# Performance work log

Measured on AMD Instinct MI355X. Metric: run time of the kernel, lower is better.

Reference implementation:

```python
import jax, jax.numpy as jnp
import numpy as np

# icosphere level 6
NV = 40962   # vertices
NF = 81920   # faces
B = 16
CIN = 32
COUT = 32
NCOEFF = 4


def _spmm(rows, cols, vals, nrows, x):
    """Sparse (COO) @ dense over the vertex/face axis.
    x: [B, C, N] -> out: [B, C, nrows].
    """
    # gather columns, scale by nonzero values, scatter-add into rows
    g = x.transpose(2, 0, 1)[cols] * vals[:, None, None]   # [nnz, B, C]
    out = jax.ops.segment_sum(g, rows, num_segments=nrows)  # [nrows, B, C]
    return out.transpose(1, 2, 0)                           # [B, C, nrows]


def setup_inputs() -> dict:
    key = jax.random.key(0)
    ks = jax.random.split(key, 10)
    x = jax.random.normal(ks[0], (B, CIN, NV), dtype=jnp.float32)

    # G: [3*NF, NV], 3 nnz per row (3 vertices per face), component-major rows
    g_nnz = 3 * NF * 3
    G_rows = jnp.repeat(jnp.arange(3 * NF, dtype=jnp.int32), 3)
    G_cols = jax.random.randint(ks[1], (g_nnz,), 0, NV, dtype=jnp.int32)
    G_vals = jax.random.normal(ks[2], (g_nnz,), dtype=jnp.float32) * 0.5

    # L: [NV, NV], ~7 nnz per row (vertex valence + self)
    l_nnz = NV * 7
    L_rows = jnp.repeat(jnp.arange(NV, dtype=jnp.int32), 7)
    L_cols = jax.random.randint(ks[3], (l_nnz,), 0, NV, dtype=jnp.int32)
    L_vals = jax.random.normal(ks[4], (l_nnz,), dtype=jnp.float32) * 0.5

    # F2V: [NV, NF], ~6 faces per vertex, averaging weights
    f_nnz = NV * 6
    F2V_rows = jnp.repeat(jnp.arange(NV, dtype=jnp.int32), 6)
    F2V_cols = jax.random.randint(ks[5], (f_nnz,), 0, NF, dtype=jnp.int32)
    F2V_vals = jnp.full((f_nnz,), 1.0 / 6.0, dtype=jnp.float32)

    # per-face east-west / north-south tangent vectors: [NF, 3]
    EW = jax.random.normal(ks[6], (NF, 3), dtype=jnp.float32)
    NS = jax.random.normal(ks[7], (NF, 3), dtype=jnp.float32)

    stdv = 1.0 / np.sqrt(CIN * NCOEFF)
    coeffs = jax.random.uniform(ks[8], (COUT, CIN, NCOEFF), dtype=jnp.float32,
                                minval=-stdv, maxval=stdv)
    bias = jax.random.uniform(ks[9], (COUT,), dtype=jnp.float32,
                              minval=-stdv, maxval=stdv)

    return {
        "x": x,
        "G_rows": G_rows, "G_cols": G_cols, "G_vals": G_vals,
        "L_rows": L_rows, "L_cols": L_cols, "L_vals": L_vals,
        "F2V_rows": F2V_rows, "F2V_cols": F2V_cols, "F2V_vals": F2V_vals,
        "EW": EW, "NS": NS,
        "coeffs": coeffs, "bias": bias,
    }


def reference(x, G_rows, G_cols, G_vals, L_rows, L_cols, L_vals,
              F2V_rows, F2V_cols, F2V_vals, EW, NS, coeffs, bias):
    b, c, nv = x.shape
    # gradient on faces: [B,C,3*NF] -> [B,C,3,NF] -> [B,C,NF,3]
    grad_face = _spmm(G_rows, G_cols, G_vals, 3 * NF, x)
    grad_face = grad_face.reshape(b, c, 3, NF).transpose(0, 1, 3, 2)
    # Laplacian on vertices (stride=1 -> nv_prev = nv)
    laplacian = _spmm(L_rows, L_cols, L_vals, NV, x)
    identity = x  # x[..., :nv_prev] with nv_prev == nv
    # project face gradients onto EW / NS frames
    grad_face_ew = jnp.sum(grad_face * EW, axis=-1)  # [B,C,NF]
    grad_face_ns = jnp.sum(grad_face * NS, axis=-1)
    # average back to vertices
    grad_vert_ew = _spmm(F2V_rows, F2V_cols, F2V_vals, NV, grad_face_ew)
    grad_vert_ns = _spmm(F2V_rows, F2V_cols, F2V_vals, NV, grad_face_ns)
    # combine 4 features with learned per-channel coefficients
    feat = jnp.stack([identity, laplacian, grad_vert_ew, grad_vert_ns], axis=-1)  # [B,C,NV,4]
    out = jnp.einsum('bcnk,ock->bon', feat, coeffs) + bias[:, None]
    return out
```

## Files before the change

### kernel.cpp

```cpp
#include <hip/hip_runtime.h>
#include <hip/hip_bf16.h>

#define NVERT 40962
#define NFACE 81920
#define GRID_V ((NVERT + 3) / 4)
#define GRID_F (NFACE / 4)

typedef unsigned int uint;
typedef __attribute__((ext_vector_type(4))) uint  uintx4;
typedef __attribute__((ext_vector_type(4))) float floatx4;
typedef __attribute__((ext_vector_type(8))) short shortx8;

__device__ __forceinline__ uint packbf2(float a, float b) {
  uint ua = __float_as_uint(a); ua = ua + 0x7fffu + ((ua >> 16) & 1u);
  uint ub = __float_as_uint(b); ub = ub + 0x7fffu + ((ub >> 16) & 1u);
  return (ua >> 16) | (ub & 0xffff0000u);
}
__device__ __forceinline__ float2 unpackbf2(uint u) {
  float2 r;
  r.x = __uint_as_float(u << 16);
  r.y = __uint_as_float(u & 0xffff0000u);
  return r;
}
__device__ __forceinline__ short bfr(float x) {
  uint u = __float_as_uint(x);
  u = u + 0x7fffu + ((u >> 16) & 1u);
  return (short)(u >> 16);
}

__device__ __forceinline__ int swz(int blk, int nwg) {
  int q = nwg >> 3, r = nwg & 7;
  int xcd = blk & 7, idx = blk >> 3;
  return (xcd < r ? xcd * (q + 1) : r * (q + 1) + (xcd - r) * q) + idx;
}

__global__ __launch_bounds__(256) void k_transpose(const float* __restrict__ x,
                                                   uint* __restrict__ xT) {
  __shared__ float tile[32][33];
  int n0 = blockIdx.x * 32;
  int r0 = blockIdx.y * 32;
  int tx = threadIdx.x & 31;
  int ty = threadIdx.x >> 5;
#pragma unroll
  for (int i = 0; i < 32; i += 8) {
    int n = n0 + tx;
    tile[ty + i][tx] = (n < NVERT)
        ? __builtin_nontemporal_load(&x[(size_t)(r0 + ty + i) * NVERT + n]) : 0.f;
  }
  __syncthreads();
#pragma unroll
  for (int i = 0; i < 32; i += 16) {
    int nl = (threadIdx.x >> 4) + i;
    int u  = threadIdx.x & 15;
    int n  = n0 + nl;
    int ug = 16 * blockIdx.y + u;
    int up = (ug & 3) * 64 + (ug >> 4) * 4 + ((ug >> 2) & 3);
    if (n < NVERT)
      xT[(size_t)n * 256 + up] = packbf2(tile[2 * u][nl], tile[2 * u + 1][nl]);
  }
}

__global__ __launch_bounds__(256) void k_prepw(const float* __restrict__ coeffs,
                                               short* __restrict__ wsW) {
  int t = threadIdx.x;
  int ks = t >> 6, lane = t & 63;
  int bm = lane & 15, h = lane >> 4;
  const float* wp0 = coeffs + (size_t)bm * 128 + 32 * ks + 8 * h;
  shortx8 f0, f1;
#pragma unroll
  for (int j = 0; j < 8; ++j) {
    f0[j] = bfr(wp0[j]);
    f1[j] = bfr(wp0[16 * 128 + j]);
  }
  *(shortx8*)(wsW + ((size_t)(ks * 2 + 0) * 64 + lane) * 8) = f0;
  *(shortx8*)(wsW + ((size_t)(ks * 2 + 1) * 64 + lane) * 8) = f1;
}

__global__ __launch_bounds__(256) void k_faces(
    const uint* __restrict__ xT,
    const int* __restrict__ Gc, const float* __restrict__ Gv,
    const float* __restrict__ EW, const float* __restrict__ NS,
    uint* __restrict__ gf) {
  const int t = threadIdx.x, lane = t & 63;
  const int f = __builtin_amdgcn_readfirstlane(swz(blockIdx.x, GRID_F) * 4 + (t >> 6));
  const int voff = 4 * lane;

  float ea[4][2], sa[4][2];
#pragma unroll
  for (int ks = 0; ks < 4; ++ks) {
    ea[ks][0] = 0.f; ea[ks][1] = 0.f;
    sa[ks][0] = 0.f; sa[ks][1] = 0.f;
  }

#pragma unroll
  for (int comp = 0; comp < 3; ++comp) {
    const int base = comp * (3 * NFACE) + 3 * f;
    const float ewc = EW[3 * f + comp];
    const float nsc = NS[3 * f + comp];
#pragma unroll
    for (int j = 0; j < 3; ++j) {
      const int col = Gc[base + j];
      const float v = Gv[base + j];
      const float ve = v * ewc, vn = v * nsc;
      uintx4 g = *(const uintx4*)(xT + (size_t)col * 256 + voff);
#pragma unroll
      for (int ks = 0; ks < 4; ++ks) {
        float2 p = unpackbf2(g[ks]);
        ea[ks][0] = fmaf(ve, p.x, ea[ks][0]); ea[ks][1] = fmaf(ve, p.y, ea[ks][1]);
        sa[ks][0] = fmaf(vn, p.x, sa[ks][0]); sa[ks][1] = fmaf(vn, p.y, sa[ks][1]);
      }
    }
  }
  uintx4 we, wn;
#pragma unroll
  for (int ks = 0; ks < 4; ++ks) {
    we[ks] = packbf2(ea[ks][0], ea[ks][1]);
    wn[ks] = packbf2(sa[ks][0], sa[ks][1]);
  }
  uint* op = gf + (size_t)f * 512 + voff;
  *(uintx4*)op         = we;
  *(uintx4*)(op + 256) = wn;
}

__global__ __launch_bounds__(256) void k_verts(
    const uint* __restrict__ xT,
    const int* __restrict__ Lc, const float* __restrict__ Lv,
    const int* __restrict__ Fc, const float* __restrict__ Fv,
    const uint* __restrict__ gf,
    const short* __restrict__ wsW, const float* __restrict__ bias,
    float* __restrict__ out) {
  const int t = threadIdx.x, lane = t & 63;
  const int n = __builtin_amdgcn_readfirstlane(swz(blockIdx.x, GRID_V) * 4 + (t >> 6));
  if (n >= NVERT) return;
  const int h = lane >> 4, bm = lane & 15;
  const int voff = 4 * lane;

  uintx4 idw = *(const uintx4*)(xT + (size_t)n * 256 + voff);

  float lap[4][2];
#pragma unroll
  for (int ks = 0; ks < 4; ++ks) { lap[ks][0] = 0.f; lap[ks][1] = 0.f; }
#pragma unroll
  for (int j = 0; j < 7; ++j) {
    const int col = Lc[7 * n + j];
    const float v = Lv[7 * n + j];
    uintx4 g = *(const uintx4*)(xT + (size_t)col * 256 + voff);
#pragma unroll
    for (int ks = 0; ks < 4; ++ks) {
      float2 p = unpackbf2(g[ks]);
      lap[ks][0] = fmaf(v, p.x, lap[ks][0]);
      lap[ks][1] = fmaf(v, p.y, lap[ks][1]);
    }
  }

  float ea[4][2], na[4][2];
#pragma unroll
  for (int ks = 0; ks < 4; ++ks) {
    ea[ks][0] = 0.f; ea[ks][1] = 0.f;
    na[ks][0] = 0.f; na[ks][1] = 0.f;
  }
#pragma unroll
  for (int j = 0; j < 6; ++j) {
    const int fc = Fc[6 * n + j];
    const float v = Fv[6 * n + j];
    const uint* rp = gf + (size_t)fc * 512 + voff;
    uintx4 ge = *(const uintx4*)rp;
    uintx4 gn = *(const uintx4*)(rp + 256);
#pragma unroll
    for (int ks = 0; ks < 4; ++ks) {
      float2 a = unpackbf2(ge[ks]);
      float2 b = unpackbf2(gn[ks]);
      ea[ks][0] = fmaf(v, a.x, ea[ks][0]); ea[ks][1] = fmaf(v, a.y, ea[ks][1]);
      na[ks][0] = fmaf(v, b.x, na[ks][0]); na[ks][1] = fmaf(v, b.y, na[ks][1]);
    }
  }

  shortx8 afr[4];
#pragma unroll
  for (int ks = 0; ks < 4; ++ks) {
    float2 ip = unpackbf2(idw[ks]);
    shortx8 a;
    a[0] = bfr(ip.x);      a[1] = bfr(lap[ks][0]);
    a[2] = bfr(ea[ks][0]); a[3] = bfr(na[ks][0]);
    a[4] = bfr(ip.y);      a[5] = bfr(lap[ks][1]);
    a[6] = bfr(ea[ks][1]); a[7] = bfr(na[ks][1]);
    afr[ks] = a;
  }

  float b0 = bias[bm], b1 = bias[16 + bm];
  floatx4 acc0 = {b0, b0, b0, b0};
  floatx4 acc1 = {b1, b1, b1, b1};
#pragma unroll
  for (int ks = 0; ks < 4; ++ks) {
    shortx8 bf0 = *(const shortx8*)(wsW + ((size_t)(ks * 2 + 0) * 64 + lane) * 8);
    acc0 = __builtin_amdgcn_mfma_f32_16x16x32_bf16(afr[ks], bf0, acc0, 0, 0, 0);
    shortx8 bf1 = *(const shortx8*)(wsW + ((size_t)(ks * 2 + 1) * 64 + lane) * 8);
    acc1 = __builtin_amdgcn_mfma_f32_16x16x32_bf16(afr[ks], bf1, acc1, 0, 0, 0);
  }

#pragma unroll
  for (int reg = 0; reg < 4; ++reg) {
    int b = h * 4 + reg;
    out[(size_t)(b * 32 + bm) * NVERT + n]      = acc0[reg];
    out[(size_t)(b * 32 + 16 + bm) * NVERT + n] = acc1[reg];
  }
}

extern "C" void kernel_launch(void* const* d_in, const int* in_sizes, int n_in,
                              void* d_out, int out_size, void* d_ws, size_t ws_size,
                              hipStream_t stream) {
  const float* x      = (const float*)d_in[0];
  const int*   Gc     = (const int*)  d_in[2];
  const float* Gv     = (const float*)d_in[3];
  const int*   Lc     = (const int*)  d_in[5];
  const float* Lv     = (const float*)d_in[6];
  const int*   Fc     = (const int*)  d_in[8];
  const float* Fv     = (const float*)d_in[9];
  const float* EW     = (const float*)d_in[10];
  const float* NS     = (const float*)d_in[11];
  const float* coeffs = (const float*)d_in[12];
  const float* bias   = (const float*)d_in[13];
  float* out = (float*)d_out;

  uint* xT  = (uint*)d_ws;
  uint* gf  = xT + (size_t)NVERT * 256;
  short* wsW = (short*)(gf + (size_t)NFACE * 512);

  dim3 gT((NVERT + 31) / 32, 16);
  k_transpose<<<gT, 256, 0, stream>>>(x, xT);
  k_prepw<<<1, 256, 0, stream>>>(coeffs, wsW);
  k_faces<<<GRID_F, 256, 0, stream>>>(xT, Gc, Gv, EW, NS, gf);
  k_verts<<<GRID_V, 256, 0, stream>>>(xT, Lc, Lv, Fc, Fv, gf, wsW, bias, out);
}
```

Measured before the change: 479.4 us.

## Compose face-to-vertex and gradient operators into per-vertex gather weights

```diff
diff --git a/kernel.cpp b/kernel.cpp
--- a/kernel.cpp
+++ b/kernel.cpp
@@ -4,7 +4,6 @@
 #define NVERT 40962
 #define NFACE 81920
 #define GRID_V ((NVERT + 3) / 4)
-#define GRID_F (NFACE / 4)
 
 typedef unsigned int uint;
 typedef __attribute__((ext_vector_type(4))) uint  uintx4;
@@ -76,57 +75,38 @@
   *(shortx8*)(wsW + ((size_t)(ks * 2 + 1) * 64 + lane) * 8) = f1;
 }
 
-__global__ __launch_bounds__(256) void k_faces(
-    const uint* __restrict__ xT,
+__global__ __launch_bounds__(256) void k_prep(
+    const int* __restrict__ Fc, const float* __restrict__ Fv,
     const int* __restrict__ Gc, const float* __restrict__ Gv,
     const float* __restrict__ EW, const float* __restrict__ NS,
-    uint* __restrict__ gf) {
-  const int t = threadIdx.x, lane = t & 63;
-  const int f = __builtin_amdgcn_readfirstlane(swz(blockIdx.x, GRID_F) * 4 + (t >> 6));
-  const int voff = 4 * lane;
-
-  float ea[4][2], sa[4][2];
-#pragma unroll
-  for (int ks = 0; ks < 4; ++ks) {
-    ea[ks][0] = 0.f; ea[ks][1] = 0.f;
-    sa[ks][0] = 0.f; sa[ks][1] = 0.f;
-  }
-
+    int* __restrict__ cols, float* __restrict__ wew, float* __restrict__ wns) {
+  int idx = blockIdx.x * 256 + threadIdx.x;
+  if (idx >= NVERT * 6) return;
+  int n = idx / 6, j = idx - 6 * n;
+  int f = Fc[idx];
+  float wv = Fv[idx];
+  int bo = n * 64 + j * 9;
 #pragma unroll
   for (int comp = 0; comp < 3; ++comp) {
-    const int base = comp * (3 * NFACE) + 3 * f;
-    const float ewc = EW[3 * f + comp];
-    const float nsc = NS[3 * f + comp];
-#pragma unroll
-    for (int j = 0; j < 3; ++j) {
-      const int col = Gc[base + j];
-      const float v = Gv[base + j];
-      const float ve = v * ewc, vn = v * nsc;
-      uintx4 g = *(const uintx4*)(xT + (size_t)col * 256 + voff);
-#pragma unroll
-      for (int ks = 0; ks < 4; ++ks) {
-        float2 p = unpackbf2(g[ks]);
-        ea[ks][0] = fmaf(ve, p.x, ea[ks][0]); ea[ks][1] = fmaf(ve, p.y, ea[ks][1]);
-        sa[ks][0] = fmaf(vn, p.x, sa[ks][0]); sa[ks][1] = fmaf(vn, p.y, sa[ks][1]);
-      }
+    float e = wv * EW[3 * f + comp];
+    float s = wv * NS[3 * f + comp];
+    int gb = 3 * (comp * NFACE + f);
+#pragma unroll
+    for (int k = 0; k < 3; ++k) {
+      int   c  = Gc[gb + k];
+      float gv = Gv[gb + k];
+      cols[bo + comp * 3 + k] = c;
+      wew[bo + comp * 3 + k]  = e * gv;
+      wns[bo + comp * 3 + k]  = s * gv;
     }
   }
-  uintx4 we, wn;
-#pragma unroll
-  for (int ks = 0; ks < 4; ++ks) {
-    we[ks] = packbf2(ea[ks][0], ea[ks][1]);
-    wn[ks] = packbf2(sa[ks][0], sa[ks][1]);
-  }
-  uint* op = gf + (size_t)f * 512 + voff;
-  *(uintx4*)op         = we;
-  *(uintx4*)(op + 256) = wn;
-}
-
-__global__ __launch_bounds__(256) void k_verts(
+}
+
+__global__ __launch_bounds__(256) void k_vfused(
     const uint* __restrict__ xT,
     const int* __restrict__ Lc, const float* __restrict__ Lv,
-    const int* __restrict__ Fc, const float* __restrict__ Fv,
-    const uint* __restrict__ gf,
+    const int* __restrict__ cols, const float* __restrict__ wew,
+    const float* __restrict__ wns,
     const short* __restrict__ wsW, const float* __restrict__ bias,
     float* __restrict__ out) {
   const int t = threadIdx.x, lane = t & 63;
@@ -159,19 +139,20 @@
     ea[ks][0] = 0.f; ea[ks][1] = 0.f;
     na[ks][0] = 0.f; na[ks][1] = 0.f;
   }
-#pragma unroll
-  for (int j = 0; j < 6; ++j) {
-    const int fc = Fc[6 * n + j];
-    const float v = Fv[6 * n + j];
-    const uint* rp = gf + (size_t)fc * 512 + voff;
-    uintx4 ge = *(const uintx4*)rp;
-    uintx4 gn = *(const uintx4*)(rp + 256);
+  const int*   cb = cols + (size_t)n * 64;
+  const float* eb = wew  + (size_t)n * 64;
+  const float* nb = wns  + (size_t)n * 64;
+#pragma unroll 6
+  for (int j = 0; j < 54; ++j) {
+    const int   c  = cb[j];
+    const float ve = eb[j];
+    const float vn = nb[j];
+    uintx4 g = *(const uintx4*)(xT + (size_t)c * 256 + voff);
 #pragma unroll
     for (int ks = 0; ks < 4; ++ks) {
-      float2 a = unpackbf2(ge[ks]);
-      float2 b = unpackbf2(gn[ks]);
-      ea[ks][0] = fmaf(v, a.x, ea[ks][0]); ea[ks][1] = fmaf(v, a.y, ea[ks][1]);
-      na[ks][0] = fmaf(v, b.x, na[ks][0]); na[ks][1] = fmaf(v, b.y, na[ks][1]);
+      float2 p = unpackbf2(g[ks]);
+      ea[ks][0] = fmaf(ve, p.x, ea[ks][0]); ea[ks][1] = fmaf(ve, p.y, ea[ks][1]);
+      na[ks][0] = fmaf(vn, p.x, na[ks][0]); na[ks][1] = fmaf(vn, p.y, na[ks][1]);
     }
   }
 
@@ -222,13 +203,17 @@
   const float* bias   = (const float*)d_in[13];
   float* out = (float*)d_out;
 
-  uint* xT  = (uint*)d_ws;
-  uint* gf  = xT + (size_t)NVERT * 256;
-  short* wsW = (short*)(gf + (size_t)NFACE * 512);
+  uint*  xT   = (uint*)d_ws;
+  int*   cols = (int*)(xT + (size_t)NVERT * 256);
+  float* wewT = (float*)(cols + (size_t)NVERT * 64);
+  float* wnsT = wewT + (size_t)NVERT * 64;
+  short* wsW  = (short*)(wnsT + (size_t)NVERT * 64);
 
   dim3 gT((NVERT + 31) / 32, 16);
   k_transpose<<<gT, 256, 0, stream>>>(x, xT);
   k_prepw<<<1, 256, 0, stream>>>(coeffs, wsW);
-  k_faces<<<GRID_F, 256, 0, stream>>>(xT, Gc, Gv, EW, NS, gf);
-  k_verts<<<GRID_V, 256, 0, stream>>>(xT, Lc, Lv, Fc, Fv, gf, wsW, bias, out);
-}
+  k_prep<<<(NVERT * 6 + 255) / 256, 256, 0, stream>>>(Fc, Fv, Gc, Gv, EW, NS,
+                                                      cols, wewT, wnsT);
+  k_vfused<<<GRID_V, 256, 0, stream>>>(xT, Lc, Lv, cols, wewT, wnsT,
+                                       wsW, bias, out);
+}
```

Measured after the change: 589.9 us. +23.0%, slower.

## Split batch into two chunks so per-pass gather working sets fit in cache

Applied to the files above, without the earlier changes.

```diff
diff --git a/kernel.cpp b/kernel.cpp
--- a/kernel.cpp
+++ b/kernel.cpp
@@ -3,8 +3,9 @@
 
 #define NVERT 40962
 #define NFACE 81920
-#define GRID_V ((NVERT + 3) / 4)
-#define GRID_F (NFACE / 4)
+#define NPAIR_V 20481
+#define GRID_VP 5121
+#define GRID_FP 10240
 
 typedef unsigned int uint;
 typedef __attribute__((ext_vector_type(4))) uint  uintx4;
@@ -33,6 +34,7 @@
   int xcd = blk & 7, idx = blk >> 3;
   return (xcd < r ? xcd * (q + 1) : r * (q + 1) + (xcd - r) * q) + idx;
 }
+
 
 __global__ __launch_bounds__(256) void k_transpose(const float* __restrict__ x,
                                                    uint* __restrict__ xT) {
@@ -54,9 +56,11 @@
     int u  = threadIdx.x & 15;
     int n  = n0 + nl;
     int ug = 16 * blockIdx.y + u;
-    int up = (ug & 3) * 64 + (ug >> 4) * 4 + ((ug >> 2) & 3);
+    int chunk = ug >> 7;
+    int q = ((ug & 3) * 8 + ((ug >> 4) & 7)) * 4 + ((ug >> 2) & 3);
     if (n < NVERT)
-      xT[(size_t)n * 256 + up] = packbf2(tile[2 * u][nl], tile[2 * u + 1][nl]);
+      xT[(size_t)chunk * NVERT * 128 + (size_t)n * 128 + q] =
+          packbf2(tile[2 * u][nl], tile[2 * u + 1][nl]);
   }
 }
 
@@ -77,13 +81,33 @@
 }
 
 __global__ __launch_bounds__(256) void k_faces(
-    const uint* __restrict__ xT,
+    const uint* __restrict__ xTc,
     const int* __restrict__ Gc, const float* __restrict__ Gv,
     const float* __restrict__ EW, const float* __restrict__ NS,
     uint* __restrict__ gf) {
   const int t = threadIdx.x, lane = t & 63;
-  const int f = __builtin_amdgcn_readfirstlane(swz(blockIdx.x, GRID_F) * 4 + (t >> 6));
-  const int voff = 4 * lane;
+  const int p = __builtin_amdgcn_readfirstlane(swz(blockIdx.x, GRID_FP) * 4 + (t >> 6));
+  const int fA = 2 * p, fB = 2 * p + 1;
+  const int vx = (lane >> 3) & 1;
+  const int Wl = ((lane >> 4) * 8 + (lane & 7)) * 4;
+
+  int   colA[9], colB[9];
+  float veA[9], vnA[9], veB[9], vnB[9];
+#pragma unroll
+  for (int comp = 0; comp < 3; ++comp) {
+    const float eA = EW[3 * fA + comp], sA = NS[3 * fA + comp];
+    const float eB = EW[3 * fB + comp], sB = NS[3 * fB + comp];
+    const int baA = comp * (3 * NFACE) + 3 * fA;
+    const int baB = comp * (3 * NFACE) + 3 * fB;
+#pragma unroll
+    for (int k = 0; k < 3; ++k) {
+      const int i = comp * 3 + k;
+      colA[i] = Gc[baA + k];  colB[i] = Gc[baB + k];
+      const float gA = Gv[baA + k], gB = Gv[baB + k];
+      veA[i] = gA * eA; vnA[i] = gA * sA;
+      veB[i] = gB * eB; vnB[i] = gB * sB;
+    }
+  }
 
   float ea[4][2], sa[4][2];
 #pragma unroll
@@ -91,24 +115,17 @@
     ea[ks][0] = 0.f; ea[ks][1] = 0.f;
     sa[ks][0] = 0.f; sa[ks][1] = 0.f;
   }
-
-#pragma unroll
-  for (int comp = 0; comp < 3; ++comp) {
-    const int base = comp * (3 * NFACE) + 3 * f;
-    const float ewc = EW[3 * f + comp];
-    const float nsc = NS[3 * f + comp];
-#pragma unroll
-    for (int j = 0; j < 3; ++j) {
-      const int col = Gc[base + j];
-      const float v = Gv[base + j];
-      const float ve = v * ewc, vn = v * nsc;
-      uintx4 g = *(const uintx4*)(xT + (size_t)col * 256 + voff);
-#pragma unroll
-      for (int ks = 0; ks < 4; ++ks) {
-        float2 p = unpackbf2(g[ks]);
-        ea[ks][0] = fmaf(ve, p.x, ea[ks][0]); ea[ks][1] = fmaf(ve, p.y, ea[ks][1]);
-        sa[ks][0] = fmaf(vn, p.x, sa[ks][0]); sa[ks][1] = fmaf(vn, p.y, sa[ks][1]);
-      }
+#pragma unroll
+  for (int i = 0; i < 9; ++i) {
+    const int   col = vx ? colB[i] : colA[i];
+    const float ve  = vx ? veB[i]  : veA[i];
+    const float vn  = vx ? vnB[i]  : vnA[i];
+    uintx4 g = *(const uintx4*)(xTc + (size_t)col * 128 + Wl);
+#pragma unroll
+    for (int ks = 0; ks < 4; ++ks) {
+      float2 pv = unpackbf2(g[ks]);
+      ea[ks][0] = fmaf(ve, pv.x, ea[ks][0]); ea[ks][1] = fmaf(ve, pv.y, ea[ks][1]);
+      sa[ks][0] = fmaf(vn, pv.x, sa[ks][0]); sa[ks][1] = fmaf(vn, pv.y, sa[ks][1]);
     }
   }
   uintx4 we, wn;
@@ -117,39 +134,54 @@
     we[ks] = packbf2(ea[ks][0], ea[ks][1]);
     wn[ks] = packbf2(sa[ks][0], sa[ks][1]);
   }
-  uint* op = gf + (size_t)f * 512 + voff;
+  uint* op = gf + (size_t)(fA + vx) * 256 + Wl;
   *(uintx4*)op         = we;
-  *(uintx4*)(op + 256) = wn;
+  *(uintx4*)(op + 128) = wn;
 }
 
 __global__ __launch_bounds__(256) void k_verts(
-    const uint* __restrict__ xT,
+    const uint* __restrict__ xTc,
     const int* __restrict__ Lc, const float* __restrict__ Lv,
     const int* __restrict__ Fc, const float* __restrict__ Fv,
     const uint* __restrict__ gf,
     const short* __restrict__ wsW, const float* __restrict__ bias,
-    float* __restrict__ out) {
+    float* __restrict__ out, int bbase) {
   const int t = threadIdx.x, lane = t & 63;
-  const int n = __builtin_amdgcn_readfirstlane(swz(blockIdx.x, GRID_V) * 4 + (t >> 6));
-  if (n >= NVERT) return;
+  const int p = __builtin_amdgcn_readfirstlane(swz(blockIdx.x, GRID_VP) * 4 + (t >> 6));
+  if (p >= NPAIR_V) return;
+  const int nA = 2 * p, nB = 2 * p + 1;
+  const int vx = (lane >> 3) & 1;
+  const int Wl = ((lane >> 4) * 8 + (lane & 7)) * 4;
   const int h = lane >> 4, bm = lane & 15;
-  const int voff = 4 * lane;
-
-  uintx4 idw = *(const uintx4*)(xT + (size_t)n * 256 + voff);
+
+  int lcA[7], lcB[7]; float lvA[7], lvB[7];
+#pragma unroll
+  for (int j = 0; j < 7; ++j) {
+    lcA[j] = Lc[7 * nA + j]; lvA[j] = Lv[7 * nA + j];
+    lcB[j] = Lc[7 * nB + j]; lvB[j] = Lv[7 * nB + j];
+  }
+  int fcA[6], fcB[6]; float fvA[6], fvB[6];
+#pragma unroll
+  for (int j = 0; j < 6; ++j) {
+    fcA[j] = Fc[6 * nA + j]; fvA[j] = Fv[6 * nA + j];
+    fcB[j] = Fc[6 * nB + j]; fvB[j] = Fv[6 * nB + j];
+  }
+
+  uintx4 idw = *(const uintx4*)(xTc + (size_t)(nA + vx) * 128 + Wl);
 
   float lap[4][2];
 #pragma unroll
   for (int ks = 0; ks < 4; ++ks) { lap[ks][0] = 0.f; lap[ks][1] = 0.f; }
 #pragma unroll
   for (int j = 0; j < 7; ++j) {
-    const int col = Lc[7 * n + j];
-    const float v = Lv[7 * n + j];
-    uintx4 g = *(const uintx4*)(xT + (size_t)col * 256 + voff);
+    const int   col = vx ? lcB[j] : lcA[j];
+    const float v   = vx ? lvB[j] : lvA[j];
+    uintx4 g = *(const uintx4*)(xTc + (size_t)col * 128 + Wl);
 #pragma unroll
     for (int ks = 0; ks < 4; ++ks) {
-      float2 p = unpackbf2(g[ks]);
-      lap[ks][0] = fmaf(v, p.x, lap[ks][0]);
-      lap[ks][1] = fmaf(v, p.y, lap[ks][1]);
+      float2 pv = unpackbf2(g[ks]);
+      lap[ks][0] = fmaf(v, pv.x, lap[ks][0]);
+      lap[ks][1] = fmaf(v, pv.y, lap[ks][1]);
     }
   }
 
@@ -161,11 +193,11 @@
   }
 #pragma unroll
   for (int j = 0; j < 6; ++j) {
-    const int fc = Fc[6 * n + j];
-    const float v = Fv[6 * n + j];
-    const uint* rp = gf + (size_t)fc * 512 + voff;
+    const int   fc = vx ? fcB[j] : fcA[j];
+    const float v  = vx ? fvB[j] : fvA[j];
+    const uint* rp = gf + (size_t)fc * 256 + Wl;
     uintx4 ge = *(const uintx4*)rp;
-    uintx4 gn = *(const uintx4*)(rp + 256);
+    uintx4 gn = *(const uintx4*)(rp + 128);
 #pragma unroll
     for (int ks = 0; ks < 4; ++ks) {
       float2 a = unpackbf2(ge[ks]);
@@ -198,11 +230,13 @@
     acc1 = __builtin_amdgcn_mfma_f32_16x16x32_bf16(afr[ks], bf1, acc1, 0, 0, 0);
   }
 
+  const int nst = (h >> 1) ? nB : nA;
+  const int blb = 4 * (h & 1);
 #pragma unroll
   for (int reg = 0; reg < 4; ++reg) {
-    int b = h * 4 + reg;
-    out[(size_t)(b * 32 + bm) * NVERT + n]      = acc0[reg];
-    out[(size_t)(b * 32 + 16 + bm) * NVERT + n] = acc1[reg];
+    const int bg = bbase + blb + reg;
+    out[(size_t)(bg * 32 + bm) * NVERT + nst]      = acc0[reg];
+    out[(size_t)(bg * 32 + 16 + bm) * NVERT + nst] = acc1[reg];
   }
 }
 
@@ -222,13 +256,17 @@
   const float* bias   = (const float*)d_in[13];
   float* out = (float*)d_out;
 
-  uint* xT  = (uint*)d_ws;
-  uint* gf  = xT + (size_t)NVERT * 256;
-  short* wsW = (short*)(gf + (size_t)NFACE * 512);
+  uint*  xT  = (uint*)d_ws;
+  uint*  gf  = xT + (size_t)2 * NVERT * 128;
+  short* wsW = (short*)(gf + (size_t)NFACE * 256);
 
   dim3 gT((NVERT + 31) / 32, 16);
   k_transpose<<<gT, 256, 0, stream>>>(x, xT);
   k_prepw<<<1, 256, 0, stream>>>(coeffs, wsW);
-  k_faces<<<GRID_F, 256, 0, stream>>>(xT, Gc, Gv, EW, NS, gf);
-  k_verts<<<GRID_V, 256, 0, stream>>>(xT, Lc, Lv, Fc, Fv, gf, wsW, bias, out);
-}
+  for (int c = 0; c < 2; ++c) {
+    const uint* xTc = xT + (size_t)c * NVERT * 128;
+    k_faces<<<GRID_FP, 256, 0, stream>>>(xTc, Gc, Gv, EW, NS, gf);
+    k_verts<<<GRID_VP, 256, 0, stream>>>(xTc, Lc, Lv, Fc, Fv, gf, wsW, bias,
+                                         out, c * 8);
+  }
+}
```

Result: faster. 457.0 us (-4.7%).
